# Kernel tuning notes

Measured on AMD Instinct MI355X. Metric: run time of the kernel, lower is better.

Reference implementation:

```python
import jax, jax.numpy as jnp
import numpy as np

N = 8192          # num nodes
F_IN = 512        # num_features
H = 256           # hidden_dim
D = 64            # embedding_dim
E = 262144        # num edges (avg degree 32)


def setup_inputs() -> dict:
    key = jax.random.key(0)
    ks = jax.random.split(key, 6)
    x = jax.random.normal(ks[0], (N, F_IN), dtype=jnp.float32)
    adj_rows = jax.random.randint(ks[1], (E,), 0, N)
    adj_cols = jax.random.randint(ks[2], (E,), 0, N)
    adj_vals = jax.random.uniform(ks[3], (E,), dtype=jnp.float32)
    W1 = jax.random.normal(ks[4], (F_IN, H), dtype=jnp.float32) / np.sqrt(F_IN)
    b1 = jnp.zeros((H,), dtype=jnp.float32)
    W2 = jax.random.normal(ks[5], (H, D), dtype=jnp.float32) / np.sqrt(H)
    b2 = jnp.zeros((D,), dtype=jnp.float32)
    return {"x": x, "adj_rows": adj_rows, "adj_cols": adj_cols,
            "adj_vals": adj_vals, "W1": W1, "b1": b1, "W2": W2, "b2": b2}


def _spmm(rows, cols, vals, dense):
    # sparse [N,N] @ dense [N,F] via gather + segment-sum (COO spmm)
    gathered = vals[:, None] * dense[cols]           # [E, F]
    return jax.ops.segment_sum(gathered, rows, num_segments=N)


def reference(x, adj_rows, adj_cols, adj_vals, W1, b1, W2, b2):
    # GCN layer 1: linear -> spmm -> relu (dropout is identity in eval mode)
    h = _spmm(adj_rows, adj_cols, adj_vals, x @ W1 + b1)   # [N, H]
    h = jax.nn.relu(h)
    # GCN layer 2: linear -> spmm
    z = _spmm(adj_rows, adj_cols, adj_vals, h @ W2 + b2)   # [N, D]
    # decode: sigmoid(z z^T)
    adj_rec = jax.nn.sigmoid(z @ z.T)                       # [N, N]
    return (z, adj_rec)
```

## Files before the change

kernel.cpp:

```cpp
#include <hip/hip_runtime.h>
#include <hip/hip_bf16.h>

#define NN 8192
#define FIN 512
#define HD 256
#define DD 64
#define NE 262144
#define BCAP 128

typedef __bf16 bf16_t;
typedef __bf16 bf16x8 __attribute__((ext_vector_type(8)));
typedef __bf16 bf16x4 __attribute__((ext_vector_type(4)));
typedef float f32x4 __attribute__((ext_vector_type(4)));

__global__ __launch_bounds__(256) void prep_kernel(const float* __restrict__ x, bf16_t* __restrict__ x_b,
                                                   const float* __restrict__ W1, bf16_t* __restrict__ w1t,
                                                   const float* __restrict__ W2, bf16_t* __restrict__ w2t,
                                                   int* __restrict__ deg) {
    int b = blockIdx.x;
    if (b < 4096) {
        int i = (b * 256 + threadIdx.x) * 4;
        float4 v = *reinterpret_cast<const float4*>(x + i);
        x_b[i + 0] = (bf16_t)v.x;
        x_b[i + 1] = (bf16_t)v.y;
        x_b[i + 2] = (bf16_t)v.z;
        x_b[i + 3] = (bf16_t)v.w;
    } else if (b < 4096 + 512) {
        int o = (b - 4096) * 256 + threadIdx.x;
        int r = o & 511;
        int c = o >> 9;
        w1t[o] = (bf16_t)W1[r * HD + c];
    } else if (b < 4096 + 512 + 64) {
        int o = (b - 4096 - 512) * 256 + threadIdx.x;
        int r = o & 255;
        int c = o >> 8;
        w2t[o] = (bf16_t)W2[r * DD + c];
    } else {
        int o = (b - 4096 - 512 - 64) * 256 + threadIdx.x;
        deg[o] = 0;
    }
}


__global__ void scatter_edges(const int* __restrict__ rows, const int* __restrict__ cols,
                              const float* __restrict__ vals,
                              int* __restrict__ deg, int* __restrict__ scol, float* __restrict__ sval) {
    int e = blockIdx.x * blockDim.x + threadIdx.x;
    if (e < NE) {
        int r = rows[e];
        int p = atomicAdd(&deg[r], 1);
        scol[r * BCAP + p] = cols[e];
        sval[r * BCAP + p] = vals[e];
    }
}


__global__ __launch_bounds__(256) void spmm_h_kernel(const int* __restrict__ deg,
                                                     const int* __restrict__ scol,
                                                     const float* __restrict__ sval,
                                                     const bf16_t* __restrict__ h0,
                                                     bf16_t* __restrict__ h) {
    int r = blockIdx.x;
    int wv = threadIdx.x >> 6;
    int lane = threadIdx.x & 63;
    int nd = deg[r];
    int base = r * BCAP;
    float a0 = 0.f, a1 = 0.f, a2 = 0.f, a3 = 0.f;
#pragma unroll 2
    for (int e = wv; e < nd; e += 4) {
        int c = scol[base + e];
        float v = sval[base + e];
        bf16x4 hv = *reinterpret_cast<const bf16x4*>(h0 + (size_t)c * HD + lane * 4);
        a0 += v * (float)hv[0];
        a1 += v * (float)hv[1];
        a2 += v * (float)hv[2];
        a3 += v * (float)hv[3];
    }
    __shared__ float red[4][256];
    red[wv][lane * 4 + 0] = a0;
    red[wv][lane * 4 + 1] = a1;
    red[wv][lane * 4 + 2] = a2;
    red[wv][lane * 4 + 3] = a3;
    __syncthreads();
    if (wv == 0) {
#pragma unroll
        for (int j = 0; j < 4; j++) {
            int f = lane * 4 + j;
            float s = red[0][f] + red[1][f] + red[2][f] + red[3][f];
            h[(size_t)r * HD + f] = (bf16_t)fmaxf(s, 0.f);
        }
    }
}

__global__ __launch_bounds__(256) void spmm_z_kernel(const int* __restrict__ deg,
                                                     const int* __restrict__ scol,
                                                     const float* __restrict__ sval,
                                                     const bf16_t* __restrict__ z0,
                                                     float* __restrict__ z_out,
                                                     bf16_t* __restrict__ z_b) {
    int r = blockIdx.x * 4 + (threadIdx.x >> 6);
    int lane = threadIdx.x & 63;
    int nd = deg[r];
    int base = r * BCAP;
    float acc = 0.f;
#pragma unroll 4
    for (int e = 0; e < nd; e++)
        acc += sval[base + e] * (float)z0[(size_t)scol[base + e] * DD + lane];
    z_out[(size_t)r * DD + lane] = acc;
    z_b[(size_t)r * DD + lane] = (bf16_t)acc;
}

template <int ACT, typename OutT, int MW>
__global__ __launch_bounds__(256) void gemm_bt(const bf16_t* __restrict__ A,
                                               const bf16_t* __restrict__ Bt,
                                               const float* __restrict__ bias,
                                               OutT* __restrict__ C,
                                               int M, int N, int K) {
    int wave = threadIdx.x >> 6;
    int lane = threadIdx.x & 63;
    int lr = lane & 15;
    int lq = lane >> 4;
    int m0 = blockIdx.x * (64 * MW) + wave * (16 * MW);
    int n0 = blockIdx.y * 64;

    f32x4 acc[MW][4];
#pragma unroll
    for (int i = 0; i < MW; i++)
#pragma unroll
        for (int t = 0; t < 4; t++) acc[i][t] = {0.f, 0.f, 0.f, 0.f};

    const bf16_t* Abase = A + (size_t)(m0 + lr) * K + lq * 8;
    const bf16_t* Bbase = Bt + (size_t)(n0 + lr) * K + lq * 8;

    for (int k0 = 0; k0 < K; k0 += 32) {
        bf16x8 a[MW];
#pragma unroll
        for (int i = 0; i < MW; i++)
            a[i] = *reinterpret_cast<const bf16x8*>(Abase + (size_t)i * 16 * K + k0);
#pragma unroll
        for (int t = 0; t < 4; t++) {
            bf16x8 b = *reinterpret_cast<const bf16x8*>(Bbase + (size_t)t * 16 * K + k0);
#pragma unroll
            for (int i = 0; i < MW; i++)
                acc[i][t] = __builtin_amdgcn_mfma_f32_16x16x32_bf16(a[i], b, acc[i][t], 0, 0, 0);
        }
    }

    if (ACT == 2) {
        __shared__ float ldsT[256 / 64 * 16 * MW][65];
        int rbase = wave * 16 * MW;
#pragma unroll
        for (int i = 0; i < MW; i++)
#pragma unroll
            for (int t = 0; t < 4; t++)
#pragma unroll
                for (int r = 0; r < 4; r++) {
                    float v = acc[i][t][r];
                    v = 1.f / (1.f + __expf(-v));
                    ldsT[rbase + i * 16 + lq * 4 + r][t * 16 + lr] = v;
                }
        int c4 = (lane & 15) * 4;
        int rr = lane >> 4;
#pragma unroll
        for (int j = 0; j < 4 * MW; j++) {
            int row_l = rbase + j * 4 + rr;
            f32x4 v = *reinterpret_cast<const f32x4*>(&ldsT[row_l][c4]);
            size_t gaddr = (size_t)(blockIdx.x * (64 * MW) + row_l) * N + n0 + c4;
            *reinterpret_cast<f32x4*>(&C[gaddr]) = v;
        }
    } else {
#pragma unroll
        for (int i = 0; i < MW; i++) {
#pragma unroll
            for (int t = 0; t < 4; t++) {
                int col = n0 + t * 16 + lr;
                float bv = bias ? bias[col] : 0.f;
#pragma unroll
                for (int r = 0; r < 4; r++) {
                    int row = m0 + i * 16 + lq * 4 + r;
                    C[(size_t)row * N + col] = (OutT)(acc[i][t][r] + bv);
                }
            }
        }
    }
}


extern "C" void kernel_launch(void* const* d_in, const int* in_sizes, int n_in,
                              void* d_out, int out_size, void* d_ws, size_t ws_size,
                              hipStream_t stream) {
    const float* x   = (const float*)d_in[0];
    const int* rows  = (const int*)d_in[1];
    const int* cols  = (const int*)d_in[2];
    const float* vals = (const float*)d_in[3];
    const float* W1  = (const float*)d_in[4];
    const float* b1  = (const float*)d_in[5];
    const float* W2  = (const float*)d_in[6];
    const float* b2  = (const float*)d_in[7];

    float* out_z   = (float*)d_out;
    float* out_adj = out_z + (size_t)NN * DD;

    char* ws = (char*)d_ws;
    size_t off = 0;
    auto alloc = [&](size_t bytes) { void* p = ws + off; off += (bytes + 255) & ~(size_t)255; return p; };
    bf16_t* x_b   = (bf16_t*)alloc((size_t)NN * FIN * 2);
    bf16_t* w1t   = (bf16_t*)alloc((size_t)HD * FIN * 2);
    bf16_t* w2t   = (bf16_t*)alloc((size_t)DD * HD * 2);
    bf16_t* h0    = (bf16_t*)alloc((size_t)NN * HD * 2);
    bf16_t* h_b   = (bf16_t*)alloc((size_t)NN * HD * 2);
    bf16_t* z0    = (bf16_t*)alloc((size_t)NN * DD * 2);
    bf16_t* z_b   = (bf16_t*)alloc((size_t)NN * DD * 2);
    int* deg      = (int*)alloc((size_t)NN * 4);
    int* scol     = (int*)alloc((size_t)NN * BCAP * 4);
    float* sval   = (float*)alloc((size_t)NN * BCAP * 4);

    prep_kernel<<<4096 + 512 + 64 + 32, 256, 0, stream>>>(x, x_b, W1, w1t, W2, w2t, deg);

    scatter_edges<<<NE / 256, 256, 0, stream>>>(rows, cols, vals, deg, scol, sval);

    gemm_bt<0, bf16_t, 1><<<dim3(NN / 64, HD / 64), 256, 0, stream>>>(x_b, w1t, b1, h0, NN, HD, FIN);

    spmm_h_kernel<<<NN, 256, 0, stream>>>(deg, scol, sval, h0, h_b);

    gemm_bt<0, bf16_t, 1><<<dim3(NN / 64, DD / 64), 256, 0, stream>>>(h_b, w2t, b2, z0, NN, DD, HD);

    spmm_z_kernel<<<NN / 4, 256, 0, stream>>>(deg, scol, sval, z0, out_z, z_b);

    gemm_bt<2, float, 2><<<dim3(NN / 128, NN / 64), 256, 0, stream>>>(z_b, z_b, nullptr, out_adj, NN, NN, DD);
}
```

Baseline: 383.5 us.

## Fuse edge scatter into GEMM1 launch and vectorize prep and SpMM stores

Merges the edge-bucketing scatter kernel and the first GEMM into one launch, with the block index choosing the role, which removes a launch and lets the two independent pieces of work overlap. The prep kernel now converts eight x elements per thread and writes packed bf16 vectors for the transposed weights and the degree reset. The h SpMM output is written as one bf16x4 store, and the z SpMM is remapped to 16 lanes per row with 4-wide loads and vector stores. Overall runtime is dominated by the dense N×N sigmoid GEMM, which is unchanged, so the total effect is likely small.

Result: no change. 387.7 us (+1.1%).

```diff
diff --git a/kernel.cpp b/kernel.cpp
--- a/kernel.cpp
+++ b/kernel.cpp
@@ -18,39 +18,81 @@
                                                    const float* __restrict__ W2, bf16_t* __restrict__ w2t,
                                                    int* __restrict__ deg) {
     int b = blockIdx.x;
-    if (b < 4096) {
-        int i = (b * 256 + threadIdx.x) * 4;
-        float4 v = *reinterpret_cast<const float4*>(x + i);
-        x_b[i + 0] = (bf16_t)v.x;
-        x_b[i + 1] = (bf16_t)v.y;
-        x_b[i + 2] = (bf16_t)v.z;
-        x_b[i + 3] = (bf16_t)v.w;
-    } else if (b < 4096 + 512) {
-        int o = (b - 4096) * 256 + threadIdx.x;
-        int r = o & 511;
-        int c = o >> 9;
-        w1t[o] = (bf16_t)W1[r * HD + c];
-    } else if (b < 4096 + 512 + 64) {
-        int o = (b - 4096 - 512) * 256 + threadIdx.x;
-        int r = o & 255;
-        int c = o >> 8;
-        w2t[o] = (bf16_t)W2[r * DD + c];
+    if (b < 2048) {
+        int i = (b * 256 + threadIdx.x) * 8;
+        float4 v0 = *reinterpret_cast<const float4*>(x + i);
+        float4 v1 = *reinterpret_cast<const float4*>(x + i + 4);
+        bf16x8 o = {(bf16_t)v0.x, (bf16_t)v0.y, (bf16_t)v0.z, (bf16_t)v0.w,
+                    (bf16_t)v1.x, (bf16_t)v1.y, (bf16_t)v1.z, (bf16_t)v1.w};
+        *reinterpret_cast<bf16x8*>(x_b + i) = o;
+    } else if (b < 2048 + 128) {
+        int o4 = ((b - 2048) * 256 + threadIdx.x) * 4;
+        int r = o4 & 511;
+        int c = o4 >> 9;
+        bf16x4 o = {(bf16_t)W1[(r + 0) * HD + c], (bf16_t)W1[(r + 1) * HD + c],
+                    (bf16_t)W1[(r + 2) * HD + c], (bf16_t)W1[(r + 3) * HD + c]};
+        *reinterpret_cast<bf16x4*>(w1t + o4) = o;
+    } else if (b < 2048 + 128 + 16) {
+        int o4 = ((b - 2048 - 128) * 256 + threadIdx.x) * 4;
+        int r = o4 & 255;
+        int c = o4 >> 8;
+        bf16x4 o = {(bf16_t)W2[(r + 0) * DD + c], (bf16_t)W2[(r + 1) * DD + c],
+                    (bf16_t)W2[(r + 2) * DD + c], (bf16_t)W2[(r + 3) * DD + c]};
+        *reinterpret_cast<bf16x4*>(w2t + o4) = o;
     } else {
-        int o = (b - 4096 - 512 - 64) * 256 + threadIdx.x;
-        deg[o] = 0;
-    }
-}
-
-
-__global__ void scatter_edges(const int* __restrict__ rows, const int* __restrict__ cols,
-                              const float* __restrict__ vals,
-                              int* __restrict__ deg, int* __restrict__ scol, float* __restrict__ sval) {
-    int e = blockIdx.x * blockDim.x + threadIdx.x;
-    if (e < NE) {
+        int o = ((b - 2048 - 128 - 16) * 256 + threadIdx.x) * 4;
+        *reinterpret_cast<int4*>(deg + o) = {0, 0, 0, 0};
+    }
+}
+
+__global__ __launch_bounds__(256) void gemm1_scatter(const bf16_t* __restrict__ A,
+                                                     const bf16_t* __restrict__ Bt,
+                                                     const float* __restrict__ bias,
+                                                     bf16_t* __restrict__ C,
+                                                     const int* __restrict__ rows, const int* __restrict__ cols,
+                                                     const float* __restrict__ vals,
+                                                     int* __restrict__ deg, int* __restrict__ scol,
+                                                     float* __restrict__ sval) {
+    int b = blockIdx.x;
+    if (b >= 512) {
+        int e = (b - 512) * 256 + threadIdx.x;
         int r = rows[e];
         int p = atomicAdd(&deg[r], 1);
         scol[r * BCAP + p] = cols[e];
         sval[r * BCAP + p] = vals[e];
+        return;
+    }
+    const int K = FIN, N = HD;
+    int wave = threadIdx.x >> 6;
+    int lane = threadIdx.x & 63;
+    int lr = lane & 15;
+    int lq = lane >> 4;
+    int m0 = (b & 127) * 64 + wave * 16;
+    int n0 = (b >> 7) * 64;
+
+    f32x4 acc[4];
+#pragma unroll
+    for (int t = 0; t < 4; t++) acc[t] = {0.f, 0.f, 0.f, 0.f};
+
+    const bf16_t* Abase = A + (size_t)(m0 + lr) * K + lq * 8;
+    const bf16_t* Bbase = Bt + (size_t)(n0 + lr) * K + lq * 8;
+    for (int k0 = 0; k0 < K; k0 += 32) {
+        bf16x8 a = *reinterpret_cast<const bf16x8*>(Abase + k0);
+#pragma unroll
+        for (int t = 0; t < 4; t++) {
+            bf16x8 bb = *reinterpret_cast<const bf16x8*>(Bbase + (size_t)t * 16 * K + k0);
+            acc[t] = __builtin_amdgcn_mfma_f32_16x16x32_bf16(a, bb, acc[t], 0, 0, 0);
+        }
+    }
+#pragma unroll
+    for (int t = 0; t < 4; t++) {
+        int col = n0 + t * 16 + lr;
+        float bv = bias[col];
+#pragma unroll
+        for (int r = 0; r < 4; r++) {
+            int row = m0 + lq * 4 + r;
+            C[(size_t)row * N + col] = (bf16_t)(acc[t][r] + bv);
+        }
     }
 }
 
@@ -83,12 +125,12 @@
     red[wv][lane * 4 + 3] = a3;
     __syncthreads();
     if (wv == 0) {
-#pragma unroll
-        for (int j = 0; j < 4; j++) {
-            int f = lane * 4 + j;
-            float s = red[0][f] + red[1][f] + red[2][f] + red[3][f];
-            h[(size_t)r * HD + f] = (bf16_t)fmaxf(s, 0.f);
-        }
+        int f = lane * 4;
+        bf16x4 o = {(bf16_t)fmaxf(red[0][f + 0] + red[1][f + 0] + red[2][f + 0] + red[3][f + 0], 0.f),
+                    (bf16_t)fmaxf(red[0][f + 1] + red[1][f + 1] + red[2][f + 1] + red[3][f + 1], 0.f),
+                    (bf16_t)fmaxf(red[0][f + 2] + red[1][f + 2] + red[2][f + 2] + red[3][f + 2], 0.f),
+                    (bf16_t)fmaxf(red[0][f + 3] + red[1][f + 3] + red[2][f + 3] + red[3][f + 3], 0.f)};
+        *reinterpret_cast<bf16x4*>(h + (size_t)r * HD + f) = o;
     }
 }
 
@@ -98,16 +140,27 @@
                                                      const bf16_t* __restrict__ z0,
                                                      float* __restrict__ z_out,
                                                      bf16_t* __restrict__ z_b) {
-    int r = blockIdx.x * 4 + (threadIdx.x >> 6);
-    int lane = threadIdx.x & 63;
+    int wv = threadIdx.x >> 6;
+    int lane = threadIdx.x & 63;
+    int lq = lane >> 4;
+    int lr = lane & 15;
+    int r = blockIdx.x * 16 + wv * 4 + lq;
     int nd = deg[r];
     int base = r * BCAP;
-    float acc = 0.f;
-#pragma unroll 4
-    for (int e = 0; e < nd; e++)
-        acc += sval[base + e] * (float)z0[(size_t)scol[base + e] * DD + lane];
-    z_out[(size_t)r * DD + lane] = acc;
-    z_b[(size_t)r * DD + lane] = (bf16_t)acc;
+    float a0 = 0.f, a1 = 0.f, a2 = 0.f, a3 = 0.f;
+    for (int e = 0; e < nd; e++) {
+        int c = scol[base + e];
+        float v = sval[base + e];
+        bf16x4 zv = *reinterpret_cast<const bf16x4*>(z0 + (size_t)c * DD + lr * 4);
+        a0 += v * (float)zv[0];
+        a1 += v * (float)zv[1];
+        a2 += v * (float)zv[2];
+        a3 += v * (float)zv[3];
+    }
+    f32x4 of = {a0, a1, a2, a3};
+    *reinterpret_cast<f32x4*>(z_out + (size_t)r * DD + lr * 4) = of;
+    bf16x4 ob = {(bf16_t)a0, (bf16_t)a1, (bf16_t)a2, (bf16_t)a3};
+    *reinterpret_cast<bf16x4*>(z_b + (size_t)r * DD + lr * 4) = ob;
 }
 
 template <int ACT, typename OutT, int MW>
@@ -215,17 +268,16 @@
     int* scol     = (int*)alloc((size_t)NN * BCAP * 4);
     float* sval   = (float*)alloc((size_t)NN * BCAP * 4);
 
-    prep_kernel<<<4096 + 512 + 64 + 32, 256, 0, stream>>>(x, x_b, W1, w1t, W2, w2t, deg);
-
-    scatter_edges<<<NE / 256, 256, 0, stream>>>(rows, cols, vals, deg, scol, sval);
-
-    gemm_bt<0, bf16_t, 1><<<dim3(NN / 64, HD / 64), 256, 0, stream>>>(x_b, w1t, b1, h0, NN, HD, FIN);
+    prep_kernel<<<2048 + 128 + 16 + 8, 256, 0, stream>>>(x, x_b, W1, w1t, W2, w2t, deg);
+
+    gemm1_scatter<<<512 + 1024, 256, 0, stream>>>(x_b, w1t, b1, h0,
+                                                  rows, cols, vals, deg, scol, sval);
 
     spmm_h_kernel<<<NN, 256, 0, stream>>>(deg, scol, sval, h0, h_b);
 
     gemm_bt<0, bf16_t, 1><<<dim3(NN / 64, DD / 64), 256, 0, stream>>>(h_b, w2t, b2, z0, NN, DD, HD);
 
-    spmm_z_kernel<<<NN / 4, 256, 0, stream>>>(deg, scol, sval, z0, out_z, z_b);
+    spmm_z_kernel<<<NN / 16, 256, 0, stream>>>(deg, scol, sval, z0, out_z, z_b);
 
     gemm_bt<2, float, 2><<<dim3(NN / 128, NN / 64), 256, 0, stream>>>(z_b, z_b, nullptr, out_adj, NN, NN, DD);
 }
```
